# Kernel optimization log

Measured on AMD Instinct MI355X. Metric: run time of the kernel, lower is better.

Reference implementation:

```python
import jax, jax.numpy as jnp
import numpy as np

B, T, D, F, E = 4, 2048, 1024, 2048, 16  # batch, seq, hidden, intermediate, experts


def setup_inputs() -> dict:
    key = jax.random.key(0)
    k0, k1, k2, k3 = jax.random.split(key, 4)
    x = jax.random.normal(k0, (B, T, D), dtype=jnp.float32)
    # gate: torch Linear(D, E, bias=False); store as [D, E] so logits = h @ Wg
    Wg = jax.random.normal(k1, (D, E), dtype=jnp.float32) * 0.02
    # experts: kaiming_uniform(a=sqrt(5)) -> U(-1/sqrt(fan_in), 1/sqrt(fan_in))
    W1 = jax.random.uniform(k2, (E, D, F), minval=-1.0, maxval=1.0, dtype=jnp.float32) / np.sqrt(D)
    W2 = jax.random.uniform(k3, (E, F, D), minval=-1.0, maxval=1.0, dtype=jnp.float32) / np.sqrt(F)
    return {"x": x, "Wg": Wg, "W1": W1, "W2": W2}


def reference(x, Wg, W1, W2):
    b, t, d = x.shape
    e = Wg.shape[1]
    h = x.reshape(-1, d)                     # [N, D], N = b*t tokens
    n = h.shape[0]

    # --- gate: top-2 routing with fp32 softmax over the 2 selected logits ---
    logits = h @ Wg                          # [N, E]
    scores, idx = jax.lax.top_k(logits, 2)   # [N, 2]
    scores = jax.nn.softmax(scores.astype(jnp.float32), axis=-1).astype(x.dtype)

    # dense combine weights [N, E]: weight of expert e for each token (0 if not routed)
    combine = jnp.zeros((n, e), dtype=x.dtype).at[
        jnp.arange(n)[:, None], idx
    ].add(scores)

    # --- dispatch/combine: scan over experts, weight-accumulate outputs ---
    # Mathematically identical to the masked-loop original: tokens not routed
    # to expert e contribute with weight 0.
    def step(acc, params):
        W1e, W2e, w = params                  # [D,F], [F,D], [N]
        out = jax.nn.silu(h @ W1e) @ W2e      # [N, D]
        return acc + w[:, None] * out, None

    y, _ = jax.lax.scan(step, jnp.zeros_like(h), (W1, W2, combine.T))
    return y.reshape(b, t, d)
```

## Files before the change

kernel.cpp:

```cpp
#include <hip/hip_runtime.h>
#include <hip/hip_bf16.h>

#define NTOK 8192
#define DDIM 1024
#define FDIM 2048
#define NEXP 16
#define CAP   1280
#define CAPRG 80

#define WS_COUNTS 0
#define WS_TOKL   4096
#define WS_WGTL   (4096 + NTOK*NEXP*4)
#define WS_POS    (4096 + 2*NTOK*NEXP*4)
#define WS_TW     (4096 + 2*NTOK*NEXP*4 + NTOK*8)
#define WS2_XG   (size_t)(2u<<20)
#define WS2_W1   (size_t)(42u<<20)
#define WS2_W2   (size_t)(106u<<20)
#define WS2_UG   (size_t)(170u<<20)

typedef short bf16x8 __attribute__((ext_vector_type(8)));
typedef float f32x4  __attribute__((ext_vector_type(4)));

__device__ __forceinline__ unsigned short f2bf(float f) {
  unsigned int u = __builtin_bit_cast(unsigned int, f);
  u += 0x7fffu + ((u >> 16) & 1u);
  return (unsigned short)(u >> 16);
}
__device__ __forceinline__ unsigned int pk2(float a, float b) {
  return (unsigned int)f2bf(a) | ((unsigned int)f2bf(b) << 16);
}
__device__ __forceinline__ float bf2f(unsigned int u) {
  return __builtin_bit_cast(float, u << 16);
}
__device__ __forceinline__ float silu_f(float s) {
  return s / (1.f + __expf(-s));
}
__device__ __forceinline__ void gld_lds16(const void* g, void* l) {
  __builtin_amdgcn_global_load_lds((const __attribute__((address_space(1))) void*)g,
                                   (__attribute__((address_space(3))) void*)l, 16, 0, 0);
}

__global__ __launch_bounds__(1024) void gate_kernel(
    const float* __restrict__ x, const float* __restrict__ Wg,
    int* __restrict__ counts, int* __restrict__ tokl, float* __restrict__ wgtl,
    int* __restrict__ pos, float* __restrict__ tw) {
  __shared__ float WgT[NEXP][DDIM];
  __shared__ int   se[32];
  __shared__ float swt[32];
  __shared__ int   sbase[16];
  int tid = threadIdx.x;
#pragma unroll
  for (int i = 0; i < 4; ++i) {
    int i4 = i * 1024 + tid;
    float4 v = ((const float4*)Wg)[i4];
    int k = i4 >> 2;
    int e0 = (i4 * 4) & 15;
    WgT[e0][k] = v.x; WgT[e0 + 1][k] = v.y;
    WgT[e0 + 2][k] = v.z; WgT[e0 + 3][k] = v.w;
  }
  __syncthreads();

  int wid = tid >> 6, lane = tid & 63;
  int tok = blockIdx.x * 16 + wid;
  const float* xr = x + (size_t)tok * DDIM;
  float xv[16];
#pragma unroll
  for (int j = 0; j < 16; ++j) xv[j] = xr[lane + 64 * j];
  float lg[NEXP];
#pragma unroll
  for (int e = 0; e < NEXP; ++e) {
    float s = 0.f;
#pragma unroll
    for (int j = 0; j < 16; ++j) s += xv[j] * WgT[e][lane + 64 * j];
#pragma unroll
    for (int off = 32; off > 0; off >>= 1) s += __shfl_xor(s, off);
    lg[e] = s;
  }
  int e0 = 0; float b0 = lg[0];
#pragma unroll
  for (int e = 1; e < NEXP; ++e) if (lg[e] > b0) { b0 = lg[e]; e0 = e; }
  int e1 = -1; float b1 = -3.4e38f;
#pragma unroll
  for (int e = 0; e < NEXP; ++e) if (e != e0 && lg[e] > b1) { b1 = lg[e]; e1 = e; }
  float t = expf(b1 - b0);
  float w0 = 1.f / (1.f + t);
  float w1 = t / (1.f + t);
  if (lane == 0) {
    se[wid * 2] = e0;  swt[wid * 2] = w0;
    se[wid * 2 + 1] = e1;  swt[wid * 2 + 1] = w1;
  }
  __syncthreads();

  if (tid < 16) {
    int cnt = 0;
#pragma unroll
    for (int i = 0; i < 32; ++i) cnt += (se[i] == tid) ? 1 : 0;
    sbase[tid] = cnt ? atomicAdd(&counts[tid * 16], cnt) : 0;
    int slot = sbase[tid];
    for (int i = 0; i < 32; ++i) {
      if (se[i] == tid) {
        int tk = blockIdx.x * 16 + (i >> 1);
        float w = swt[i];
        if (slot < CAP) { tokl[tid * NTOK + slot] = tk; wgtl[tid * NTOK + slot] = w; }
        pos[tk * 2 + (i & 1)] = (slot < CAP) ? (tid * CAP + slot) : -1;
        tw[tk * 2 + (i & 1)] = w;
        slot++;
      }
    }
  }
}

__global__ __launch_bounds__(256) void convert_w2(
    const float* __restrict__ W1, const float* __restrict__ W2,
    unsigned short* __restrict__ W1s, unsigned short* __restrict__ W2s) {
  __shared__ float tile[32][133];
  int b = blockIdx.x;
  bool isw2 = b >= 8192;
  int bb = isw2 ? b - 8192 : b;
  int e = bb >> 9;
  int r = bb & 511;
  int t = threadIdx.x;
  const float* src;
  int kk, cb, C;
  if (!isw2) {
    kk = r >> 4; cb = r & 15; C = FDIM;
    src = W1 + ((size_t)e << 21) + (size_t)(kk * 32) * FDIM + cb * 128;
  } else {
    kk = r >> 3; cb = r & 7; C = DDIM;
    src = W2 + ((size_t)e << 21) + (size_t)(kk * 32) * DDIM + cb * 128;
  }
  int c4 = (t & 31) * 4, rr0 = t >> 5;
#pragma unroll
  for (int rd = 0; rd < 4; ++rd) {
    int rr = rr0 + rd * 8;
    float4 v = *(const float4*)(src + (size_t)rr * C + c4);
    tile[rr][c4] = v.x; tile[rr][c4 + 1] = v.y;
    tile[rr][c4 + 2] = v.z; tile[rr][c4 + 3] = v.w;
  }
  __syncthreads();
  int w = t >> 6, lane = t & 63, llo = lane & 15, lhi = lane >> 4;
#pragma unroll
  for (int u = 0; u < 2; ++u) {
    int c2 = w * 2 + u;
    float v[8];
#pragma unroll
    for (int j = 0; j < 8; ++j) {
      int row = isw2 ? (4 * lhi + (j & 3) + 16 * (j >> 2)) : (lhi * 8 + j);
      v[j] = tile[row][c2 * 16 + llo];
    }
    uint4 o;
    o.x = pk2(v[0], v[1]); o.y = pk2(v[2], v[3]);
    o.z = pk2(v[4], v[5]); o.w = pk2(v[6], v[7]);
    size_t gid = isw2 ? (((size_t)e * 64 + kk) * 64 + (cb * 8 + c2))
                      : (((size_t)e * 128 + (cb * 8 + c2)) * 32 + kk);
    *(uint4*)((isw2 ? W2s : W1s) + (gid << 9) + lane * 8) = o;
  }
}

__global__ __launch_bounds__(512) void gather_x(
    const float* __restrict__ x, const int* __restrict__ counts,
    const int* __restrict__ tokl, unsigned short* __restrict__ Xg) {
  int chunk = blockIdx.x * 8 + (threadIdx.x >> 6);
  int lane = threadIdx.x & 63, llo = lane & 15, lhi = lane >> 4;
  int kb = chunk & 31;
  int rg = (chunk >> 5) % CAPRG;
  int e = chunk / (CAPRG * 32);
  int cnt = min(counts[e * 16], CAP);
  int slot = rg * 16 + llo;
  uint4 o = {0u, 0u, 0u, 0u};
  if (slot < cnt) {
    int tok = tokl[e * NTOK + slot];
    const float* p = x + (size_t)tok * DDIM + kb * 32 + lhi * 8;
    float4 a = *(const float4*)p, b2 = *(const float4*)(p + 4);
    o.x = pk2(a.x, a.y); o.y = pk2(a.z, a.w);
    o.z = pk2(b2.x, b2.y); o.w = pk2(b2.z, b2.w);
  }
  *(uint4*)(Xg + ((size_t)chunk << 9) + lane * 8) = o;
}

__global__ __launch_bounds__(512, 4) void g1(
    const unsigned short* __restrict__ W1s, const unsigned short* __restrict__ Xg,
    const int* __restrict__ counts, unsigned short* __restrict__ Ug) {
  int id = blockIdx.x;
  int e = ((id & 7) << 1) | ((id >> 3) & 1);
  int rest = id >> 4;
  int ft = rest & 15;
  int tt = rest >> 4;
  int cnt = min(counts[e * 16], CAP);
  if (tt * 256 >= cnt) return;

  extern __shared__ char smem[];
  int tid = threadIdx.x, wid = tid >> 6, lane = tid & 63;
  int llo = lane & 15, lhi = lane >> 4;
  int fm = wid >> 2, wn = wid & 3;

  f32x4 acc[4][4];
#pragma unroll
  for (int i = 0; i < 4; ++i)
#pragma unroll
    for (int j = 0; j < 4; ++j) acc[i][j] = (f32x4){0.f, 0.f, 0.f, 0.f};

  const size_t abase = ((size_t)e * 128 + ft * 8) * 32;
  const size_t bbase = ((size_t)e * CAPRG + tt * 16) * 32;

  const int c0 = wid * 3;
  const unsigned short* gsrc0;
  const unsigned short* gsrc1;
  const unsigned short* gsrc2;
  {
    int c = c0;
    gsrc0 = (c < 8) ? W1s + ((abase + (size_t)c * 32) << 9) + lane * 8
                    : Xg + ((bbase + (size_t)(c - 8) * 32) << 9) + lane * 8;
    c = c0 + 1;
    gsrc1 = (c < 8) ? W1s + ((abase + (size_t)c * 32) << 9) + lane * 8
                    : Xg + ((bbase + (size_t)(c - 8) * 32) << 9) + lane * 8;
    c = c0 + 2;
    gsrc2 = (c < 8) ? W1s + ((abase + (size_t)c * 32) << 9) + lane * 8
                    : Xg + ((bbase + (size_t)(c - 8) * 32) << 9) + lane * 8;
  }
  const int doff0 = (c0 + 0) * 1024;
  const int doff1 = (c0 + 1) * 1024;
  const int doff2 = (c0 + 2) * 1024;
  const int lo16 = lane * 16;
  const int aoff = fm * 4096;
  const int boff = 8192 + wn * 4096;

#define G1_STAGE(ROT)                                                           \
  {                                                                             \
    char* dst = smem + (ROT);                                                   \
    gld_lds16(gsrc0, dst + doff0);                                              \
    gld_lds16(gsrc1, dst + doff1);                                              \
    gld_lds16(gsrc2, dst + doff2);                                              \
    gsrc0 += 512; gsrc1 += 512; gsrc2 += 512;                                   \
  }

  G1_STAGE(0);
  G1_STAGE(24576);
  asm volatile("s_waitcnt vmcnt(3)" ::: "memory");
  __builtin_amdgcn_s_barrier();
  int rotw = 49152, rotr = 0;
  for (int t = 0; t < 32; ++t) {
    if (t + 2 < 32) G1_STAGE(rotw);
    const char* bufc = smem + rotr;
    bf16x8 af[4], bx[4];
#pragma unroll
    for (int fi = 0; fi < 4; ++fi)
      af[fi] = *(const bf16x8*)(bufc + aoff + fi * 1024 + lo16);
#pragma unroll
    for (int ti = 0; ti < 4; ++ti)
      bx[ti] = *(const bf16x8*)(bufc + boff + ti * 1024 + lo16);
#pragma unroll
    for (int fi = 0; fi < 4; ++fi)
#pragma unroll
      for (int ti = 0; ti < 4; ++ti)
        acc[fi][ti] = __builtin_amdgcn_mfma_f32_16x16x32_bf16(af[fi], bx[ti], acc[fi][ti], 0, 0, 0);
    asm volatile("s_waitcnt lgkmcnt(0)" ::: "memory");
    __builtin_amdgcn_sched_barrier(0);
    if (t + 2 < 32) {
      asm volatile("s_waitcnt vmcnt(3)" ::: "memory");
    } else if (t + 1 < 32) {
      asm volatile("s_waitcnt vmcnt(0)" ::: "memory");
    }
    __builtin_amdgcn_s_barrier();
    rotw = (rotw == 49152) ? 0 : rotw + 24576;
    rotr = (rotr == 49152) ? 0 : rotr + 24576;
  }

#pragma unroll
  for (int ti = 0; ti < 4; ++ti) {
    int rg = tt * 16 + wn * 4 + ti;
#pragma unroll
    for (int p = 0; p < 2; ++p) {
      int fo = ft * 4 + fm * 2 + p;
      uint4 v;
      v.x = pk2(silu_f(acc[2 * p][ti][0]), silu_f(acc[2 * p][ti][1]));
      v.y = pk2(silu_f(acc[2 * p][ti][2]), silu_f(acc[2 * p][ti][3]));
      v.z = pk2(silu_f(acc[2 * p + 1][ti][0]), silu_f(acc[2 * p + 1][ti][1]));
      v.w = pk2(silu_f(acc[2 * p + 1][ti][2]), silu_f(acc[2 * p + 1][ti][3]));
      *(uint4*)(Ug + ((((size_t)e * CAPRG + rg) * 64 + fo) << 9) + lane * 8) = v;
    }
  }
}

__global__ __launch_bounds__(512, 4) void g2(
    const unsigned short* __restrict__ W2s, const unsigned short* __restrict__ Ug,
    const int* __restrict__ counts, unsigned short* __restrict__ Yp) {
  int id = blockIdx.x;
  int e = ((id & 7) << 1) | ((id >> 3) & 1);
  int rest = id >> 4;
  int dt = rest & 7;
  int tt = rest >> 3;
  int cnt = min(counts[e * 16], CAP);
  int tb0 = tt * 256;
  if (tb0 >= cnt) return;

  extern __shared__ char smem[];
  int tid = threadIdx.x;
  int wid = tid >> 6, lane = tid & 63, llo = lane & 15, lhi = lane >> 4;
  int dm = wid >> 2, wn = wid & 3;

  f32x4 acc[4][4];
#pragma unroll
  for (int i = 0; i < 4; ++i)
#pragma unroll
    for (int j = 0; j < 4; ++j) acc[i][j] = (f32x4){0.f, 0.f, 0.f, 0.f};

  const size_t bbase = ((size_t)e * CAPRG + tt * 16) * 64;

  const int c0 = wid * 3;
  const unsigned short* gsrc0;
  const unsigned short* gsrc1;
  const unsigned short* gsrc2;
  int st0, st1, st2;
  {
    int c = c0;
    if (c < 8) { gsrc0 = W2s + ((((size_t)e * 64) * 64 + dt * 8 + c) << 9) + lane * 8; st0 = 32768; }
    else       { gsrc0 = Ug + ((bbase + (size_t)(c - 8) * 64) << 9) + lane * 8; st0 = 512; }
    c = c0 + 1;
    if (c < 8) { gsrc1 = W2s + ((((size_t)e * 64) * 64 + dt * 8 + c) << 9) + lane * 8; st1 = 32768; }
    else       { gsrc1 = Ug + ((bbase + (size_t)(c - 8) * 64) << 9) + lane * 8; st1 = 512; }
    c = c0 + 2;
    if (c < 8) { gsrc2 = W2s + ((((size_t)e * 64) * 64 + dt * 8 + c) << 9) + lane * 8; st2 = 32768; }
    else       { gsrc2 = Ug + ((bbase + (size_t)(c - 8) * 64) << 9) + lane * 8; st2 = 512; }
  }
  const int doff0 = (c0 + 0) * 1024;
  const int doff1 = (c0 + 1) * 1024;
  const int doff2 = (c0 + 2) * 1024;
  const int lo16 = lane * 16;
  const int aoff = dm * 4096;
  const int boff = 8192 + wn * 4096;

#define G2_STAGE(ROT)                                                           \
  {                                                                             \
    char* dst = smem + (ROT);                                                   \
    gld_lds16(gsrc0, dst + doff0);                                              \
    gld_lds16(gsrc1, dst + doff1);                                              \
    gld_lds16(gsrc2, dst + doff2);                                              \
    gsrc0 += st0; gsrc1 += st1; gsrc2 += st2;                                   \
  }

  G2_STAGE(0);
  G2_STAGE(24576);
  asm volatile("s_waitcnt vmcnt(3)" ::: "memory");
  __builtin_amdgcn_s_barrier();
  int rotw = 49152, rotr = 0;
  for (int t = 0; t < 64; ++t) {
    if (t + 2 < 64) G2_STAGE(rotw);
    const char* bufc = smem + rotr;
    bf16x8 aw[4], bu[4];
#pragma unroll
    for (int di = 0; di < 4; ++di)
      aw[di] = *(const bf16x8*)(bufc + aoff + di * 1024 + lo16);
#pragma unroll
    for (int ti = 0; ti < 4; ++ti)
      bu[ti] = *(const bf16x8*)(bufc + boff + ti * 1024 + lo16);
#pragma unroll
    for (int di = 0; di < 4; ++di)
#pragma unroll
      for (int ti = 0; ti < 4; ++ti)
        acc[di][ti] = __builtin_amdgcn_mfma_f32_16x16x32_bf16(aw[di], bu[ti], acc[di][ti], 0, 0, 0);
    asm volatile("s_waitcnt lgkmcnt(0)" ::: "memory");
    __builtin_amdgcn_sched_barrier(0);
    if (t + 2 < 64) {
      asm volatile("s_waitcnt vmcnt(3)" ::: "memory");
    } else if (t + 1 < 64) {
      asm volatile("s_waitcnt vmcnt(0)" ::: "memory");
    }
    __builtin_amdgcn_s_barrier();
    rotw = (rotw == 49152) ? 0 : rotw + 24576;
    rotr = (rotr == 49152) ? 0 : rotr + 24576;
  }

#pragma unroll
  for (int di = 0; di < 4; ++di)
#pragma unroll
    for (int ti = 0; ti < 4; ++ti) {
      int slot = tb0 + wn * 64 + ti * 16 + llo;
      int d = dt * 128 + dm * 64 + di * 16 + 4 * lhi;
      uint2 v;
      v.x = pk2(acc[di][ti][0], acc[di][ti][1]);
      v.y = pk2(acc[di][ti][2], acc[di][ti][3]);
      *(uint2*)(Yp + (((size_t)e * CAP + slot) << 10) + d) = v;
    }
}

__global__ __launch_bounds__(256) void combine_k(
    const unsigned short* __restrict__ Yp, const int* __restrict__ pos,
    const float* __restrict__ tw, float* __restrict__ out) {
  int gid = blockIdx.x * 256 + threadIdx.x;
  int tok = gid >> 7, oct = gid & 127;
  int p0 = pos[tok * 2], p1 = pos[tok * 2 + 1];
  float w0 = tw[tok * 2], w1 = tw[tok * 2 + 1];
  float r[8];
#pragma unroll
  for (int j = 0; j < 8; ++j) r[j] = 0.f;
  if (p0 >= 0) {
    uint4 a = *(const uint4*)(Yp + (((size_t)p0) << 10) + (oct << 3));
    unsigned int w[4] = {a.x, a.y, a.z, a.w};
#pragma unroll
    for (int h = 0; h < 4; ++h) {
      r[2 * h]     += w0 * bf2f(w[h] & 0xffffu);
      r[2 * h + 1] += w0 * bf2f(w[h] >> 16);
    }
  }
  if (p1 >= 0) {
    uint4 a = *(const uint4*)(Yp + (((size_t)p1) << 10) + (oct << 3));
    unsigned int w[4] = {a.x, a.y, a.z, a.w};
#pragma unroll
    for (int h = 0; h < 4; ++h) {
      r[2 * h]     += w1 * bf2f(w[h] & 0xffffu);
      r[2 * h + 1] += w1 * bf2f(w[h] >> 16);
    }
  }
  float4 o0 = {r[0], r[1], r[2], r[3]}, o1 = {r[4], r[5], r[6], r[7]};
  float* dst = out + ((size_t)tok << 10) + (oct << 3);
  *(float4*)dst = o0;
  *(float4*)(dst + 4) = o1;
}

extern "C" void kernel_launch(void* const* d_in, const int* in_sizes, int n_in,
                              void* d_out, int out_size, void* d_ws, size_t ws_size,
                              hipStream_t stream) {
  const float* x  = (const float*)d_in[0];
  const float* Wg = (const float*)d_in[1];
  const float* W1 = (const float*)d_in[2];
  const float* W2 = (const float*)d_in[3];
  float* out = (float*)d_out;

  int*   counts = (int*)((char*)d_ws + WS_COUNTS);
  int*   tokl   = (int*)((char*)d_ws + WS_TOKL);
  float* wgtl   = (float*)((char*)d_ws + WS_WGTL);
  int*   pos    = (int*)((char*)d_ws + WS_POS);
  float* tw     = (float*)((char*)d_ws + WS_TW);
  unsigned short* XgN = (unsigned short*)((char*)d_ws + WS2_XG);
  unsigned short* W1n = (unsigned short*)((char*)d_ws + WS2_W1);
  unsigned short* W2n = (unsigned short*)((char*)d_ws + WS2_W2);
  unsigned short* UgN = (unsigned short*)((char*)d_ws + WS2_UG);

  hipMemsetAsync(counts, 0, 1024, stream);

  gate_kernel<<<NTOK / 16, 1024, 0, stream>>>(x, Wg, counts, tokl, wgtl, pos, tw);
  convert_w2<<<16384, 256, 0, stream>>>(W1, W2, W1n, W2n);
  gather_x<<<5120, 512, 0, stream>>>(x, counts, tokl, XgN);

  hipFuncSetAttribute((const void*)g1,
                      hipFuncAttributeMaxDynamicSharedMemorySize, 73728);
  hipFuncSetAttribute((const void*)g2,
                      hipFuncAttributeMaxDynamicSharedMemorySize, 73728);
  g1<<<NEXP * 16 * 5, 512, 73728, stream>>>(W1n, XgN, counts, UgN);
  g2<<<NEXP * 8 * 5, 512, 73728, stream>>>(W2n, UgN, counts, XgN );
  combine_k<<<4096, 256, 0, stream>>>(XgN , pos, tw, out);
}
```

Measured before the change: 342.2 us.

## Halve token tile in expert GEMMs and deepen LDS pipeline to four stages

Both expert GEMM kernels shrink the token tile from 256 to 128 tokens per block, doubling the grid and halving per-wave accumulators and B-operand loads. The shared-memory ring goes from three 24 KB stages to four 16 KB stages, with updated waitcnt thresholds for prefetching three stages ahead. The aim is finer load balance across variable per-expert token counts, less wasted padding work, and better latency hiding. The cost is lower arithmetic intensity per block, since the weight tiles are reloaded twice as often.

Result: slower. 357.6 us (+4.5%).

```diff
diff --git a/kernel.cpp b/kernel.cpp
--- a/kernel.cpp
+++ b/kernel.cpp
@@ -187,26 +187,25 @@
   int ft = rest & 15;
   int tt = rest >> 4;
   int cnt = min(counts[e * 16], CAP);
-  if (tt * 256 >= cnt) return;
+  if (tt * 128 >= cnt) return;
 
   extern __shared__ char smem[];
   int tid = threadIdx.x, wid = tid >> 6, lane = tid & 63;
   int llo = lane & 15, lhi = lane >> 4;
   int fm = wid >> 2, wn = wid & 3;
 
-  f32x4 acc[4][4];
+  f32x4 acc[4][2];
 #pragma unroll
   for (int i = 0; i < 4; ++i)
 #pragma unroll
-    for (int j = 0; j < 4; ++j) acc[i][j] = (f32x4){0.f, 0.f, 0.f, 0.f};
+    for (int j = 0; j < 2; ++j) acc[i][j] = (f32x4){0.f, 0.f, 0.f, 0.f};
 
   const size_t abase = ((size_t)e * 128 + ft * 8) * 32;
-  const size_t bbase = ((size_t)e * CAPRG + tt * 16) * 32;
-
-  const int c0 = wid * 3;
+  const size_t bbase = ((size_t)e * CAPRG + tt * 8) * 32;
+
+  const int c0 = wid * 2;
   const unsigned short* gsrc0;
   const unsigned short* gsrc1;
-  const unsigned short* gsrc2;
   {
     int c = c0;
     gsrc0 = (c < 8) ? W1s + ((abase + (size_t)c * 32) << 9) + lane * 8
@@ -214,61 +213,59 @@
     c = c0 + 1;
     gsrc1 = (c < 8) ? W1s + ((abase + (size_t)c * 32) << 9) + lane * 8
                     : Xg + ((bbase + (size_t)(c - 8) * 32) << 9) + lane * 8;
-    c = c0 + 2;
-    gsrc2 = (c < 8) ? W1s + ((abase + (size_t)c * 32) << 9) + lane * 8
-                    : Xg + ((bbase + (size_t)(c - 8) * 32) << 9) + lane * 8;
   }
   const int doff0 = (c0 + 0) * 1024;
   const int doff1 = (c0 + 1) * 1024;
-  const int doff2 = (c0 + 2) * 1024;
   const int lo16 = lane * 16;
   const int aoff = fm * 4096;
-  const int boff = 8192 + wn * 4096;
+  const int boff = 8192 + wn * 2048;
 
 #define G1_STAGE(ROT)                                                           \
   {                                                                             \
     char* dst = smem + (ROT);                                                   \
     gld_lds16(gsrc0, dst + doff0);                                              \
     gld_lds16(gsrc1, dst + doff1);                                              \
-    gld_lds16(gsrc2, dst + doff2);                                              \
-    gsrc0 += 512; gsrc1 += 512; gsrc2 += 512;                                   \
+    gsrc0 += 512; gsrc1 += 512;                                                 \
   }
 
   G1_STAGE(0);
-  G1_STAGE(24576);
-  asm volatile("s_waitcnt vmcnt(3)" ::: "memory");
+  G1_STAGE(16384);
+  G1_STAGE(32768);
+  asm volatile("s_waitcnt vmcnt(4)" ::: "memory");
   __builtin_amdgcn_s_barrier();
   int rotw = 49152, rotr = 0;
   for (int t = 0; t < 32; ++t) {
-    if (t + 2 < 32) G1_STAGE(rotw);
+    if (t + 3 < 32) G1_STAGE(rotw);
     const char* bufc = smem + rotr;
-    bf16x8 af[4], bx[4];
+    bf16x8 af[4], bx[2];
 #pragma unroll
     for (int fi = 0; fi < 4; ++fi)
       af[fi] = *(const bf16x8*)(bufc + aoff + fi * 1024 + lo16);
 #pragma unroll
-    for (int ti = 0; ti < 4; ++ti)
+    for (int ti = 0; ti < 2; ++ti)
       bx[ti] = *(const bf16x8*)(bufc + boff + ti * 1024 + lo16);
 #pragma unroll
     for (int fi = 0; fi < 4; ++fi)
 #pragma unroll
-      for (int ti = 0; ti < 4; ++ti)
+      for (int ti = 0; ti < 2; ++ti)
         acc[fi][ti] = __builtin_amdgcn_mfma_f32_16x16x32_bf16(af[fi], bx[ti], acc[fi][ti], 0, 0, 0);
     asm volatile("s_waitcnt lgkmcnt(0)" ::: "memory");
     __builtin_amdgcn_sched_barrier(0);
-    if (t + 2 < 32) {
-      asm volatile("s_waitcnt vmcnt(3)" ::: "memory");
+    if (t + 3 < 32) {
+      asm volatile("s_waitcnt vmcnt(4)" ::: "memory");
+    } else if (t + 2 < 32) {
+      asm volatile("s_waitcnt vmcnt(2)" ::: "memory");
     } else if (t + 1 < 32) {
       asm volatile("s_waitcnt vmcnt(0)" ::: "memory");
     }
     __builtin_amdgcn_s_barrier();
-    rotw = (rotw == 49152) ? 0 : rotw + 24576;
-    rotr = (rotr == 49152) ? 0 : rotr + 24576;
-  }
-
-#pragma unroll
-  for (int ti = 0; ti < 4; ++ti) {
-    int rg = tt * 16 + wn * 4 + ti;
+    rotw = (rotw == 49152) ? 0 : rotw + 16384;
+    rotr = (rotr == 49152) ? 0 : rotr + 16384;
+  }
+
+#pragma unroll
+  for (int ti = 0; ti < 2; ++ti) {
+    int rg = tt * 8 + wn * 2 + ti;
 #pragma unroll
     for (int p = 0; p < 2; ++p) {
       int fo = ft * 4 + fm * 2 + p;
@@ -291,7 +288,7 @@
   int dt = rest & 7;
   int tt = rest >> 3;
   int cnt = min(counts[e * 16], CAP);
-  int tb0 = tt * 256;
+  int tb0 = tt * 128;
   if (tb0 >= cnt) return;
 
   extern __shared__ char smem[];
@@ -299,83 +296,83 @@
   int wid = tid >> 6, lane = tid & 63, llo = lane & 15, lhi = lane >> 4;
   int dm = wid >> 2, wn = wid & 3;
 
-  f32x4 acc[4][4];
+  f32x4 acc[4][2];
 #pragma unroll
   for (int i = 0; i < 4; ++i)
 #pragma unroll
-    for (int j = 0; j < 4; ++j) acc[i][j] = (f32x4){0.f, 0.f, 0.f, 0.f};
-
-  const size_t bbase = ((size_t)e * CAPRG + tt * 16) * 64;
-
-  const int c0 = wid * 3;
+    for (int j = 0; j < 2; ++j) acc[i][j] = (f32x4){0.f, 0.f, 0.f, 0.f};
+
+  const size_t bbase = ((size_t)e * CAPRG + tt * 8) * 64;
+
+  const int c0 = wid * 2;
   const unsigned short* gsrc0;
   const unsigned short* gsrc1;
-  const unsigned short* gsrc2;
-  int st0, st1, st2;
+  int st01;
   {
-    int c = c0;
-    if (c < 8) { gsrc0 = W2s + ((((size_t)e * 64) * 64 + dt * 8 + c) << 9) + lane * 8; st0 = 32768; }
-    else       { gsrc0 = Ug + ((bbase + (size_t)(c - 8) * 64) << 9) + lane * 8; st0 = 512; }
-    c = c0 + 1;
-    if (c < 8) { gsrc1 = W2s + ((((size_t)e * 64) * 64 + dt * 8 + c) << 9) + lane * 8; st1 = 32768; }
-    else       { gsrc1 = Ug + ((bbase + (size_t)(c - 8) * 64) << 9) + lane * 8; st1 = 512; }
-    c = c0 + 2;
-    if (c < 8) { gsrc2 = W2s + ((((size_t)e * 64) * 64 + dt * 8 + c) << 9) + lane * 8; st2 = 32768; }
-    else       { gsrc2 = Ug + ((bbase + (size_t)(c - 8) * 64) << 9) + lane * 8; st2 = 512; }
+    if (c0 < 8) {
+      gsrc0 = W2s + ((((size_t)e * 64) * 64 + dt * 8 + c0) << 9) + lane * 8;
+      gsrc1 = W2s + ((((size_t)e * 64) * 64 + dt * 8 + c0 + 1) << 9) + lane * 8;
+      st01 = 32768;
+    } else {
+      gsrc0 = Ug + ((bbase + (size_t)(c0 - 8) * 64) << 9) + lane * 8;
+      gsrc1 = Ug + ((bbase + (size_t)(c0 - 7) * 64) << 9) + lane * 8;
+      st01 = 512;
+    }
   }
   const int doff0 = (c0 + 0) * 1024;
   const int doff1 = (c0 + 1) * 1024;
-  const int doff2 = (c0 + 2) * 1024;
   const int lo16 = lane * 16;
   const int aoff = dm * 4096;
-  const int boff = 8192 + wn * 4096;
+  const int boff = 8192 + wn * 2048;
 
 #define G2_STAGE(ROT)                                                           \
   {                                                                             \
     char* dst = smem + (ROT);                                                   \
     gld_lds16(gsrc0, dst + doff0);                                              \
     gld_lds16(gsrc1, dst + doff1);                                              \
-    gld_lds16(gsrc2, dst + doff2);                                              \
-    gsrc0 += st0; gsrc1 += st1; gsrc2 += st2;                                   \
+    gsrc0 += st01; gsrc1 += st01;                                               \
   }
 
   G2_STAGE(0);
-  G2_STAGE(24576);
-  asm volatile("s_waitcnt vmcnt(3)" ::: "memory");
+  G2_STAGE(16384);
+  G2_STAGE(32768);
+  asm volatile("s_waitcnt vmcnt(4)" ::: "memory");
   __builtin_amdgcn_s_barrier();
   int rotw = 49152, rotr = 0;
   for (int t = 0; t < 64; ++t) {
-    if (t + 2 < 64) G2_STAGE(rotw);
+    if (t + 3 < 64) G2_STAGE(rotw);
     const char* bufc = smem + rotr;
-    bf16x8 aw[4], bu[4];
+    bf16x8 aw[4], bu[2];
 #pragma unroll
     for (int di = 0; di < 4; ++di)
       aw[di] = *(const bf16x8*)(bufc + aoff + di * 1024 + lo16);
 #pragma unroll
-    for (int ti = 0; ti < 4; ++ti)
+    for (int ti = 0; ti < 2; ++ti)
       bu[ti] = *(const bf16x8*)(bufc + boff + ti * 1024 + lo16);
 #pragma unroll
     for (int di = 0; di < 4; ++di)
 #pragma unroll
-      for (int ti = 0; ti < 4; ++ti)
+      for (int ti = 0; ti < 2; ++ti)
         acc[di][ti] = __builtin_amdgcn_mfma_f32_16x16x32_bf16(aw[di], bu[ti], acc[di][ti], 0, 0, 0);
     asm volatile("s_waitcnt lgkmcnt(0)" ::: "memory");
     __builtin_amdgcn_sched_barrier(0);
-    if (t + 2 < 64) {
-      asm volatile("s_waitcnt vmcnt(3)" ::: "memory");
+    if (t + 3 < 64) {
+      asm volatile("s_waitcnt vmcnt(4)" ::: "memory");
+    } else if (t + 2 < 64) {
+      asm volatile("s_waitcnt vmcnt(2)" ::: "memory");
     } else if (t + 1 < 64) {
       asm volatile("s_waitcnt vmcnt(0)" ::: "memory");
     }
     __builtin_amdgcn_s_barrier();
-    rotw = (rotw == 49152) ? 0 : rotw + 24576;
-    rotr = (rotr == 49152) ? 0 : rotr + 24576;
+    rotw = (rotw == 49152) ? 0 : rotw + 16384;
+    rotr = (rotr == 49152) ? 0 : rotr + 16384;
   }
 
 #pragma unroll
   for (int di = 0; di < 4; ++di)
 #pragma unroll
-    for (int ti = 0; ti < 4; ++ti) {
-      int slot = tb0 + wn * 64 + ti * 16 + llo;
+    for (int ti = 0; ti < 2; ++ti) {
+      int slot = tb0 + wn * 32 + ti * 16 + llo;
       int d = dt * 128 + dm * 64 + di * 16 + 4 * lhi;
       uint2 v;
       v.x = pk2(acc[di][ti][0], acc[di][ti][1]);
@@ -444,10 +441,10 @@
   gather_x<<<5120, 512, 0, stream>>>(x, counts, tokl, XgN);
 
   hipFuncSetAttribute((const void*)g1,
-                      hipFuncAttributeMaxDynamicSharedMemorySize, 73728);
+                      hipFuncAttributeMaxDynamicSharedMemorySize, 65536);
   hipFuncSetAttribute((const void*)g2,
-                      hipFuncAttributeMaxDynamicSharedMemorySize, 73728);
-  g1<<<NEXP * 16 * 5, 512, 73728, stream>>>(W1n, XgN, counts, UgN);
-  g2<<<NEXP * 8 * 5, 512, 73728, stream>>>(W2n, UgN, counts, XgN );
+                      hipFuncAttributeMaxDynamicSharedMemorySize, 65536);
+  g1<<<NEXP * 16 * 10, 512, 65536, stream>>>(W1n, XgN, counts, UgN);
+  g2<<<NEXP * 8 * 10, 512, 65536, stream>>>(W2n, UgN, counts, XgN );
   combine_k<<<4096, 256, 0, stream>>>(XgN , pos, tw, out);
 }
```
